# Optimization experiments

Measured on AMD Instinct MI355X. Metric: run time of the kernel, lower is better.

The kernel has to match this reference:

```python
import jax, jax.numpy as jnp
import numpy as np
from jax import lax

# Module config (matches init_kwargs)
FILTERS = 4
C, D_K, H, W = 4, 3, 128, 128   # kernel_size = [c, d, h, w]
ACT_SIZE = (3, 3, 3)            # activate_size
ACT_STRIDE = (3, 1, 1)          # activate_stride
LEAKY_ALPHA = 0.2               # tf.nn.leaky_relu default
BATCH, DEPTH = 4, 16


def setup_inputs() -> dict:
    key = jax.random.key(0)
    kx, kw, kb = jax.random.split(key, 3)
    x = jax.random.normal(kx, (BATCH, C, DEPTH, H, W), jnp.float32)
    # he_normal on the [filters,1,c,d,h,w] maps (fan_in = c*d*h*w)
    scale = np.float32(np.sqrt(2.0 / (C * D_K * H * W)))
    weight = jax.random.normal(kw, (FILTERS, 1, C, D_K, H, W), jnp.float32) * scale
    bias = jax.random.normal(kb, (FILTERS, 1, C, D_K, H, W), jnp.float32) * scale
    return {"x": x, "weight": weight, "bias": bias}


def _forward(x, weight, bias):
    # x: [B, c, D, h, w]; weight/bias: [F, 1, c, d, h, w]
    B, c, D, h, w = x.shape
    F, d = weight.shape[0], weight.shape[3]
    Dout = D - d + 1  # valid depth windows (try/except skips the out-of-range tails)

    # Sliding depth windows: [B, c, Dout, d, h, w] -> [B, Dout, c, d, h, w]
    idx = jnp.arange(Dout)[:, None] + jnp.arange(d)[None, :]
    xw = jnp.transpose(x[:, :, idx], (0, 2, 1, 3, 4, 5))

    # Per-filter affine on each window (vectorized over F and Dout):
    # a[b,f,i] = x_window[b,i] * weight[f,0] + bias[f,0]  -> [B, F, Dout, c, d, h, w]
    a = xw[:, None] * weight[:, 0][None, :, None] + bias[:, 0][None, :, None]
    a = a.reshape(B * F * Dout, c, d, h, w)

    # Non-trainable 'activate' conv: Conv3D(filters=1, kernel=ones, SAME,
    # channels_first, no bias) followed by leaky_relu(alpha=0.2)
    kern = jnp.ones((1, c) + ACT_SIZE, a.dtype)  # OIDHW
    y = lax.conv_general_dilated(
        a, kern, window_strides=ACT_STRIDE, padding='SAME',
        dimension_numbers=('NCDHW', 'OIDHW', 'NCDHW'))
    y = jax.nn.leaky_relu(y, LEAKY_ALPHA)  # [B*F*Dout, 1, dout, h, w]

    dout = y.shape[2]  # = 1 for d=3, stride 3 (SAME)
    # Concatenation over filters (axis=1) then depth (axis=2)
    return y.reshape(B, F, Dout * dout, h, w)


def reference(x, weight, bias):
    return _forward(x, weight, bias)
```

## Files before the change

### kernel.cpp

```cpp
#include <hip/hip_runtime.h>

#define HH    128
#define WW    128
#define CDIM  4
#define DK    3
#define FDIM  4
#define DEPTH 16
#define DOUT  14
#define NB    4
#define HW    (HH * WW)
#define TROWS 4
#define HROWS (TROWS + 2)
#define NTILE (HH / TROWS)
#define NIG   4

#define NW4   (FDIM * CDIM * DK * HW / 4)
#define WCONV_BLOCKS 48

typedef float nfloat4 __attribute__((ext_vector_type(4)));

__device__ __forceinline__ float bf2f(unsigned short u) {
    return __uint_as_float(((unsigned int)u) << 16);
}
__device__ __forceinline__ unsigned short f2bf_rtne(float f) {
    unsigned int u = __float_as_uint(f);
    u += 0x7FFFu + ((u >> 16) & 1u);
    return (unsigned short)(u >> 16);
}

__global__ __launch_bounds__(256) void prepass_kernel(const float4* __restrict__ bias,
                                                      const float4* __restrict__ wgt,
                                                      float4* __restrict__ bsum,
                                                      ushort4* __restrict__ w16) {
    const int blk = blockIdx.x;
    const int tid = threadIdx.x;
    if (blk < 64) {
        int idx = blk * 256 + tid;
        int f   = idx >> 12;
        int hw4 = idx & 4095;
        const float4* bp = bias + f * (CDIM * DK * (HW / 4)) + hw4;
        float4 s = make_float4(0.f, 0.f, 0.f, 0.f);
#pragma unroll
        for (int c = 0; c < CDIM; ++c)
#pragma unroll
            for (int dd = 0; dd < DK; ++dd) {
                float4 v = bp[(c * DK + dd) * (HW / 4)];
                s.x += v.x; s.y += v.y; s.z += v.z; s.w += v.w;
            }
        bsum[idx] = s;
    } else {
        const int local = blk - 64;
#pragma unroll
        for (int k = 0; k < 16; ++k) {
            int idx = local * 4096 + k * 256 + tid;
            float4 v = wgt[idx];
            ushort4 o;
            o.x = f2bf_rtne(v.x); o.y = f2bf_rtne(v.y);
            o.z = f2bf_rtne(v.z); o.w = f2bf_rtne(v.w);
            w16[idx] = o;
        }
    }
}

__global__ __launch_bounds__(256, 2) void linerconv_main(const float* __restrict__ x,
                                                         const unsigned short* __restrict__ w16,
                                                         const float* __restrict__ bsum,
                                                         float* __restrict__ out) {
    const int blk  = blockIdx.x;
    const int tile = blk & (NTILE - 1);
    const int ig   = (blk >> 5) & (NIG - 1);
    const int b    = blk >> 7;
    const int i0   = ig * 4;
    const int h0   = tile * TROWS;
    const bool full = (ig != NIG - 1);

    __shared__ float lds[4][FDIM][HROWS][WW];

    const int tid = threadIdx.x;

    if (tid < HROWS * 32) {
        const int row = tid >> 5;
        const int q   = tid & 31;
        const int g   = h0 - 1 + row;
        if (g >= 0 && g < HH) {
            const int base_hw = g * WW + q * 4;
            const float* xb = x + (b * CDIM * DEPTH + i0) * HW + base_hw;
            const unsigned short* wb = w16 + base_hw;
            if (full) {
                float4 acc[4][FDIM];
#pragma unroll
                for (int f = 0; f < FDIM; ++f) {
                    float4 bv = *(const float4*)(bsum + f * HW + base_hw);
#pragma unroll
                    for (int i2 = 0; i2 < 4; ++i2) acc[i2][f] = bv;
                }
#pragma unroll
                for (int c = 0; c < CDIM; ++c) {
                    float4 xp[6];
#pragma unroll
                    for (int j = 0; j < 6; ++j)
                        xp[j] = *(const float4*)(xb + c * (DEPTH * HW) + j * HW);
#pragma unroll
                    for (int dd = 0; dd < DK; ++dd) {
#pragma unroll
                        for (int f = 0; f < FDIM; ++f) {
                            ushort4 wu = *(const ushort4*)(wb + ((f * CDIM + c) * DK + dd) * HW);
                            float wx = bf2f(wu.x), wy = bf2f(wu.y);
                            float wz = bf2f(wu.z), ww = bf2f(wu.w);
#pragma unroll
                            for (int i2 = 0; i2 < 4; ++i2) {
                                acc[i2][f].x += xp[i2 + dd].x * wx;
                                acc[i2][f].y += xp[i2 + dd].y * wy;
                                acc[i2][f].z += xp[i2 + dd].z * wz;
                                acc[i2][f].w += xp[i2 + dd].w * ww;
                            }
                        }
                    }
                }
#pragma unroll
                for (int i2 = 0; i2 < 4; ++i2)
#pragma unroll
                    for (int f = 0; f < FDIM; ++f)
                        *(float4*)&lds[i2][f][row][q * 4] = acc[i2][f];
            } else {
                float4 acc[2][FDIM];
#pragma unroll
                for (int f = 0; f < FDIM; ++f) {
                    float4 bv = *(const float4*)(bsum + f * HW + base_hw);
                    acc[0][f] = bv;
                    acc[1][f] = bv;
                }
#pragma unroll
                for (int c = 0; c < CDIM; ++c) {
                    float4 xp[4];
#pragma unroll
                    for (int j = 0; j < 4; ++j)
                        xp[j] = *(const float4*)(xb + c * (DEPTH * HW) + j * HW);
#pragma unroll
                    for (int dd = 0; dd < DK; ++dd) {
#pragma unroll
                        for (int f = 0; f < FDIM; ++f) {
                            ushort4 wu = *(const ushort4*)(wb + ((f * CDIM + c) * DK + dd) * HW);
                            float wx = bf2f(wu.x), wy = bf2f(wu.y);
                            float wz = bf2f(wu.z), ww = bf2f(wu.w);
#pragma unroll
                            for (int i2 = 0; i2 < 2; ++i2) {
                                acc[i2][f].x += xp[i2 + dd].x * wx;
                                acc[i2][f].y += xp[i2 + dd].y * wy;
                                acc[i2][f].z += xp[i2 + dd].z * wz;
                                acc[i2][f].w += xp[i2 + dd].w * ww;
                            }
                        }
                    }
                }
#pragma unroll
                for (int i2 = 0; i2 < 2; ++i2)
#pragma unroll
                    for (int f = 0; f < FDIM; ++f)
                        *(float4*)&lds[i2][f][row][q * 4] = acc[i2][f];
            }
        } else {
            float4 z = make_float4(0.f, 0.f, 0.f, 0.f);
#pragma unroll
            for (int i2 = 0; i2 < 4; ++i2)
#pragma unroll
                for (int f = 0; f < FDIM; ++f)
                    *(float4*)&lds[i2][f][row][q * 4] = z;
        }
    }
    __syncthreads();

    auto do_quadcol = [&](int idx) {
        const int q  = idx & 31;
        const int f  = (idx >> 5) & 3;
        const int i2 = idx >> 7;
        const float* Lb = &lds[i2][f][0][0];
        float4 rs[HROWS];
#pragma unroll
        for (int g = 0; g < HROWS; ++g) {
            const float* Lr = Lb + g * WW;
            float4 m  = *(const float4*)(Lr + q * 4);
            float lft = (q > 0)  ? Lr[q * 4 - 1] : 0.f;
            float rgt = (q < 31) ? Lr[q * 4 + 4] : 0.f;
            rs[g].x = lft + m.x + m.y;
            rs[g].y = m.x + m.y + m.z;
            rs[g].z = m.y + m.z + m.w;
            rs[g].w = m.z + m.w + rgt;
        }
        float* op = out + ((b * FDIM + f) * DOUT + (i0 + i2)) * HW + h0 * WW + q * 4;
#pragma unroll
        for (int r = 0; r < TROWS; ++r) {
            nfloat4 s;
            s.x = rs[r].x + rs[r + 1].x + rs[r + 2].x;
            s.y = rs[r].y + rs[r + 1].y + rs[r + 2].y;
            s.z = rs[r].z + rs[r + 1].z + rs[r + 2].z;
            s.w = rs[r].w + rs[r + 1].w + rs[r + 2].w;
            s.x = (s.x >= 0.f) ? s.x : 0.2f * s.x;
            s.y = (s.y >= 0.f) ? s.y : 0.2f * s.y;
            s.z = (s.z >= 0.f) ? s.z : 0.2f * s.z;
            s.w = (s.w >= 0.f) ? s.w : 0.2f * s.w;
            __builtin_nontemporal_store(s, (nfloat4*)(op + r * WW));
        }
    };
    do_quadcol(tid);
    if (full) do_quadcol(tid + 256);
}

extern "C" void kernel_launch(void* const* d_in, const int* in_sizes, int n_in,
                              void* d_out, int out_size, void* d_ws, size_t ws_size,
                              hipStream_t stream) {
    const float* x    = (const float*)d_in[0];
    const float* wgt  = (const float*)d_in[1];
    const float* bias = (const float*)d_in[2];
    float* out  = (float*)d_out;

    float*          bsum = (float*)d_ws;
    unsigned short* w16  = (unsigned short*)((char*)d_ws + 65536 * 4);

    prepass_kernel<<<64 + WCONV_BLOCKS, 256, 0, stream>>>(
        (const float4*)bias, (const float4*)wgt, (float4*)bsum, (ushort4*)w16);
    linerconv_main<<<NB * NIG * NTILE, 256, 0, stream>>>(x, w16, bsum, out);
}
```

Baseline: 18.89 us.

## Split filter dimension across threads with 768-thread blocks in main kernel

Block size grows from 256 to 768 threads, and the filter loop in the first phase is spread across threads: each of 6 rows x 4 filters x 32 quads gets its own thread instead of one thread handling all four filters. Previously only 192 threads did the affine stage and the stencil phase ran twice per thread. Each thread now holds fewer accumulators and more wavefronts are in flight to hide memory latency. The cost is that each x value is loaded four times, once per filter thread, rather than reused in registers. It also adds some idle threads in the stencil phase.

New measurement: 21.13 us. 1.12x slower.

```diff
diff --git a/kernel.cpp b/kernel.cpp
--- a/kernel.cpp
+++ b/kernel.cpp
@@ -14,7 +14,6 @@
 #define NTILE (HH / TROWS)
 #define NIG   4
 
-#define NW4   (FDIM * CDIM * DK * HW / 4)
 #define WCONV_BLOCKS 48
 
 typedef float nfloat4 __attribute__((ext_vector_type(4)));
@@ -62,7 +61,7 @@
     }
 }
 
-__global__ __launch_bounds__(256, 2) void linerconv_main(const float* __restrict__ x,
+__global__ __launch_bounds__(768, 4) void linerconv_main(const float* __restrict__ x,
                                                          const unsigned short* __restrict__ w16,
                                                          const float* __restrict__ bsum,
                                                          float* __restrict__ out) {
@@ -77,133 +76,113 @@
     __shared__ float lds[4][FDIM][HROWS][WW];
 
     const int tid = threadIdx.x;
-
-    if (tid < HROWS * 32) {
-        const int row = tid >> 5;
-        const int q   = tid & 31;
-        const int g   = h0 - 1 + row;
-        if (g >= 0 && g < HH) {
-            const int base_hw = g * WW + q * 4;
-            const float* xb = x + (b * CDIM * DEPTH + i0) * HW + base_hw;
-            const unsigned short* wb = w16 + base_hw;
-            if (full) {
-                float4 acc[4][FDIM];
-#pragma unroll
-                for (int f = 0; f < FDIM; ++f) {
-                    float4 bv = *(const float4*)(bsum + f * HW + base_hw);
-#pragma unroll
-                    for (int i2 = 0; i2 < 4; ++i2) acc[i2][f] = bv;
-                }
-#pragma unroll
-                for (int c = 0; c < CDIM; ++c) {
-                    float4 xp[6];
-#pragma unroll
-                    for (int j = 0; j < 6; ++j)
-                        xp[j] = *(const float4*)(xb + c * (DEPTH * HW) + j * HW);
-#pragma unroll
-                    for (int dd = 0; dd < DK; ++dd) {
-#pragma unroll
-                        for (int f = 0; f < FDIM; ++f) {
-                            ushort4 wu = *(const ushort4*)(wb + ((f * CDIM + c) * DK + dd) * HW);
-                            float wx = bf2f(wu.x), wy = bf2f(wu.y);
-                            float wz = bf2f(wu.z), ww = bf2f(wu.w);
-#pragma unroll
-                            for (int i2 = 0; i2 < 4; ++i2) {
-                                acc[i2][f].x += xp[i2 + dd].x * wx;
-                                acc[i2][f].y += xp[i2 + dd].y * wy;
-                                acc[i2][f].z += xp[i2 + dd].z * wz;
-                                acc[i2][f].w += xp[i2 + dd].w * ww;
-                            }
-                        }
+    const int row = tid >> 7;
+    const int rem = tid & 127;
+    const int f   = rem >> 5;
+    const int q   = rem & 31;
+    const int g   = h0 - 1 + row;
+
+    if (g >= 0 && g < HH) {
+        const int base_hw = g * WW + q * 4;
+        const float* xb = x + (b * CDIM * DEPTH + i0) * HW + base_hw;
+        const unsigned short* wb = w16 + ((f * CDIM) * DK) * HW + base_hw;
+        float4 bv = *(const float4*)(bsum + f * HW + base_hw);
+        if (full) {
+            float4 acc[4];
+#pragma unroll
+            for (int i2 = 0; i2 < 4; ++i2) acc[i2] = bv;
+#pragma unroll
+            for (int c = 0; c < CDIM; ++c) {
+                float4 xp[6];
+#pragma unroll
+                for (int j = 0; j < 6; ++j)
+                    xp[j] = *(const float4*)(xb + c * (DEPTH * HW) + j * HW);
+#pragma unroll
+                for (int dd = 0; dd < DK; ++dd) {
+                    ushort4 wu = *(const ushort4*)(wb + (c * DK + dd) * HW);
+                    float wx = bf2f(wu.x), wy = bf2f(wu.y);
+                    float wz = bf2f(wu.z), ww = bf2f(wu.w);
+#pragma unroll
+                    for (int i2 = 0; i2 < 4; ++i2) {
+                        acc[i2].x += xp[i2 + dd].x * wx;
+                        acc[i2].y += xp[i2 + dd].y * wy;
+                        acc[i2].z += xp[i2 + dd].z * wz;
+                        acc[i2].w += xp[i2 + dd].w * ww;
                     }
                 }
-#pragma unroll
-                for (int i2 = 0; i2 < 4; ++i2)
-#pragma unroll
-                    for (int f = 0; f < FDIM; ++f)
-                        *(float4*)&lds[i2][f][row][q * 4] = acc[i2][f];
-            } else {
-                float4 acc[2][FDIM];
-#pragma unroll
-                for (int f = 0; f < FDIM; ++f) {
-                    float4 bv = *(const float4*)(bsum + f * HW + base_hw);
-                    acc[0][f] = bv;
-                    acc[1][f] = bv;
-                }
-#pragma unroll
-                for (int c = 0; c < CDIM; ++c) {
-                    float4 xp[4];
-#pragma unroll
-                    for (int j = 0; j < 4; ++j)
-                        xp[j] = *(const float4*)(xb + c * (DEPTH * HW) + j * HW);
-#pragma unroll
-                    for (int dd = 0; dd < DK; ++dd) {
-#pragma unroll
-                        for (int f = 0; f < FDIM; ++f) {
-                            ushort4 wu = *(const ushort4*)(wb + ((f * CDIM + c) * DK + dd) * HW);
-                            float wx = bf2f(wu.x), wy = bf2f(wu.y);
-                            float wz = bf2f(wu.z), ww = bf2f(wu.w);
-#pragma unroll
-                            for (int i2 = 0; i2 < 2; ++i2) {
-                                acc[i2][f].x += xp[i2 + dd].x * wx;
-                                acc[i2][f].y += xp[i2 + dd].y * wy;
-                                acc[i2][f].z += xp[i2 + dd].z * wz;
-                                acc[i2][f].w += xp[i2 + dd].w * ww;
-                            }
-                        }
+            }
+#pragma unroll
+            for (int i2 = 0; i2 < 4; ++i2)
+                *(float4*)&lds[i2][f][row][q * 4] = acc[i2];
+        } else {
+            float4 acc[2];
+            acc[0] = bv; acc[1] = bv;
+#pragma unroll
+            for (int c = 0; c < CDIM; ++c) {
+                float4 xp[4];
+#pragma unroll
+                for (int j = 0; j < 4; ++j)
+                    xp[j] = *(const float4*)(xb + c * (DEPTH * HW) + j * HW);
+#pragma unroll
+                for (int dd = 0; dd < DK; ++dd) {
+                    ushort4 wu = *(const ushort4*)(wb + (c * DK + dd) * HW);
+                    float wx = bf2f(wu.x), wy = bf2f(wu.y);
+                    float wz = bf2f(wu.z), ww = bf2f(wu.w);
+#pragma unroll
+                    for (int i2 = 0; i2 < 2; ++i2) {
+                        acc[i2].x += xp[i2 + dd].x * wx;
+                        acc[i2].y += xp[i2 + dd].y * wy;
+                        acc[i2].z += xp[i2 + dd].z * wz;
+                        acc[i2].w += xp[i2 + dd].w * ww;
                     }
                 }
-#pragma unroll
-                for (int i2 = 0; i2 < 2; ++i2)
-#pragma unroll
-                    for (int f = 0; f < FDIM; ++f)
-                        *(float4*)&lds[i2][f][row][q * 4] = acc[i2][f];
-            }
-        } else {
-            float4 z = make_float4(0.f, 0.f, 0.f, 0.f);
-#pragma unroll
-            for (int i2 = 0; i2 < 4; ++i2)
-#pragma unroll
-                for (int f = 0; f < FDIM; ++f)
-                    *(float4*)&lds[i2][f][row][q * 4] = z;
+            }
+#pragma unroll
+            for (int i2 = 0; i2 < 2; ++i2)
+                *(float4*)&lds[i2][f][row][q * 4] = acc[i2];
+        }
+    } else {
+        float4 z = make_float4(0.f, 0.f, 0.f, 0.f);
+#pragma unroll
+        for (int i2 = 0; i2 < 4; ++i2)
+            *(float4*)&lds[i2][f][row][q * 4] = z;
+    }
+    __syncthreads();
+
+    if (tid < 512) {
+        const int uq = tid & 31;
+        const int uf = (tid >> 5) & 3;
+        const int i2 = tid >> 7;
+        if (full || i2 < 2) {
+            const float* Lb = &lds[i2][uf][0][0];
+            float4 rs[HROWS];
+#pragma unroll
+            for (int gg = 0; gg < HROWS; ++gg) {
+                const float* Lr = Lb + gg * WW;
+                float4 m  = *(const float4*)(Lr + uq * 4);
+                float lft = (uq > 0)  ? Lr[uq * 4 - 1] : 0.f;
+                float rgt = (uq < 31) ? Lr[uq * 4 + 4] : 0.f;
+                rs[gg].x = lft + m.x + m.y;
+                rs[gg].y = m.x + m.y + m.z;
+                rs[gg].z = m.y + m.z + m.w;
+                rs[gg].w = m.z + m.w + rgt;
+            }
+            float* op = out + ((b * FDIM + uf) * DOUT + (i0 + i2)) * HW + h0 * WW + uq * 4;
+#pragma unroll
+            for (int r = 0; r < TROWS; ++r) {
+                nfloat4 s;
+                s.x = rs[r].x + rs[r + 1].x + rs[r + 2].x;
+                s.y = rs[r].y + rs[r + 1].y + rs[r + 2].y;
+                s.z = rs[r].z + rs[r + 1].z + rs[r + 2].z;
+                s.w = rs[r].w + rs[r + 1].w + rs[r + 2].w;
+                s.x = (s.x >= 0.f) ? s.x : 0.2f * s.x;
+                s.y = (s.y >= 0.f) ? s.y : 0.2f * s.y;
+                s.z = (s.z >= 0.f) ? s.z : 0.2f * s.z;
+                s.w = (s.w >= 0.f) ? s.w : 0.2f * s.w;
+                __builtin_nontemporal_store(s, (nfloat4*)(op + r * WW));
+            }
         }
     }
-    __syncthreads();
-
-    auto do_quadcol = [&](int idx) {
-        const int q  = idx & 31;
-        const int f  = (idx >> 5) & 3;
-        const int i2 = idx >> 7;
-        const float* Lb = &lds[i2][f][0][0];
-        float4 rs[HROWS];
-#pragma unroll
-        for (int g = 0; g < HROWS; ++g) {
-            const float* Lr = Lb + g * WW;
-            float4 m  = *(const float4*)(Lr + q * 4);
-            float lft = (q > 0)  ? Lr[q * 4 - 1] : 0.f;
-            float rgt = (q < 31) ? Lr[q * 4 + 4] : 0.f;
-            rs[g].x = lft + m.x + m.y;
-            rs[g].y = m.x + m.y + m.z;
-            rs[g].z = m.y + m.z + m.w;
-            rs[g].w = m.z + m.w + rgt;
-        }
-        float* op = out + ((b * FDIM + f) * DOUT + (i0 + i2)) * HW + h0 * WW + q * 4;
-#pragma unroll
-        for (int r = 0; r < TROWS; ++r) {
-            nfloat4 s;
-            s.x = rs[r].x + rs[r + 1].x + rs[r + 2].x;
-            s.y = rs[r].y + rs[r + 1].y + rs[r + 2].y;
-            s.z = rs[r].z + rs[r + 1].z + rs[r + 2].z;
-            s.w = rs[r].w + rs[r + 1].w + rs[r + 2].w;
-            s.x = (s.x >= 0.f) ? s.x : 0.2f * s.x;
-            s.y = (s.y >= 0.f) ? s.y : 0.2f * s.y;
-            s.z = (s.z >= 0.f) ? s.z : 0.2f * s.z;
-            s.w = (s.w >= 0.f) ? s.w : 0.2f * s.w;
-            __builtin_nontemporal_store(s, (nfloat4*)(op + r * WW));
-        }
-    };
-    do_quadcol(tid);
-    if (full) do_quadcol(tid + 256);
 }
 
 extern "C" void kernel_launch(void* const* d_in, const int* in_sizes, int n_in,
@@ -219,5 +198,5 @@
 
     prepass_kernel<<<64 + WCONV_BLOCKS, 256, 0, stream>>>(
         (const float4*)bias, (const float4*)wgt, (float4*)bsum, (ushort4*)w16);
-    linerconv_main<<<NB * NIG * NTILE, 256, 0, stream>>>(x, w16, bsum, out);
-}
+    linerconv_main<<<NB * NIG * NTILE, 768, 0, stream>>>(x, w16, bsum, out);
+}
```
